# Kernel tuning notes

Hardware: AMD Instinct MI355X
Metric: run time of the kernel (lower is better)

Reference implementation:

```python
import jax, jax.numpy as jnp
import numpy as np

N_TOKENS, D_MODEL, D_HIDDEN, TOPK = 4096, 1024, 16384, 64


def setup_inputs() -> dict:
    key = jax.random.key(0)
    k0, k1, k2 = jax.random.split(key, 3)
    x = jax.random.normal(k0, (N_TOKENS, D_MODEL), dtype=jnp.float32)
    # kaiming_uniform_(a=sqrt(5)) -> bound = 1/sqrt(fan_in)
    lim_enc = 1.0 / np.sqrt(D_MODEL)
    W_enc = jax.random.uniform(k1, (D_MODEL, D_HIDDEN), jnp.float32, -lim_enc, lim_enc)
    b_enc = jnp.zeros((D_HIDDEN,), jnp.float32)
    lim_dec = 1.0 / np.sqrt(D_HIDDEN)
    W_dec = jax.random.uniform(k2, (D_HIDDEN, D_MODEL), jnp.float32, -lim_dec, lim_dec)
    # normalize_decoder=True: rows (one per feature) are unit-normalized in-place
    # under no_grad in torch, so we pre-normalize the parameter here.
    W_dec = W_dec / jnp.clip(jnp.linalg.norm(W_dec, axis=1, keepdims=True), 1e-8, None)
    b_dec = jnp.zeros((D_MODEL,), jnp.float32)
    return {"x": x, "W_enc": W_enc, "b_enc": b_enc, "W_dec": W_dec, "b_dec": b_dec, "k": TOPK}


def reference(x, W_enc, b_enc, W_dec, b_dec, k):
    # encode
    pre = x @ W_enc + b_enc                     # [N, d_hidden]
    # ReLU activation (config in ('relu','topk'))
    z = jax.nn.relu(pre)
    # TopK on |z| along feature dim, scatter original values back
    _, idx = jax.lax.top_k(jnp.abs(z), k)        # [N, k]
    rows = jnp.arange(z.shape[0])[:, None]       # [N, 1]
    z_sparse = jnp.zeros_like(z).at[rows, idx].set(jnp.take_along_axis(z, idx, axis=-1))
    # decode (W_dec rows are already unit-norm; torch re-normalizes under no_grad)
    y = z_sparse @ W_dec + b_dec                # [N, d_model]
    return y
```

## Files before the change

### kernel.cpp

```cpp
#include <hip/hip_runtime.h>

typedef unsigned short ushort_t;
typedef unsigned short ushort8 __attribute__((ext_vector_type(8)));
typedef __bf16 bf16x8 __attribute__((ext_vector_type(8)));
typedef float f32x4 __attribute__((ext_vector_type(4)));

#define N_TOKENS 4096
#define D_MODEL  1024
#define D_HIDDEN 16384
#define TOPK     64
#define DELTA    0.03f
#define RCAP     128

__device__ __forceinline__ float bf2f(ushort_t u) {
  union { unsigned u; float f; } c; c.u = ((unsigned)u) << 16; return c.f;
}
__device__ __forceinline__ ushort_t f2bf(float f) {
  union { float f; unsigned u; } c; c.f = f;
  unsigned x = c.u;
  unsigned r = (x + 0x7FFFu + ((x >> 16) & 1u)) >> 16;
  return (ushort_t)r;
}

typedef __attribute__((address_space(1))) void GV;
typedef __attribute__((address_space(3))) void LV;
__device__ __forceinline__ void llds16(const void* g, void* l) {
  __builtin_amdgcn_global_load_lds((GV*)g, (LV*)l, 16, 0, 0);
}

__global__ __launch_bounds__(256) void cast_x_kernel(
    const float* __restrict__ in, ushort_t* __restrict__ out) {
  const int i = (blockIdx.x * 256 + threadIdx.x) * 4;
  float4 v = *(const float4*)&in[i];
  ushort4 o;
  o.x = f2bf(v.x); o.y = f2bf(v.y); o.z = f2bf(v.z); o.w = f2bf(v.w);
  *(ushort4*)&out[i] = o;
}

__global__ __launch_bounds__(256) void cast_wdec_kernel(
    const float* __restrict__ in, ushort_t* __restrict__ out) {
  const int i = (blockIdx.x * 256 + threadIdx.x) * 8;
  float4 v0 = *(const float4*)&in[i];
  float4 v1 = *(const float4*)&in[i + 4];
  ushort8 o;
  o[0] = f2bf(v0.x); o[1] = f2bf(v0.y); o[2] = f2bf(v0.z); o[3] = f2bf(v0.w);
  o[4] = f2bf(v1.x); o[5] = f2bf(v1.y); o[6] = f2bf(v1.z); o[7] = f2bf(v1.w);
  *(ushort8*)&out[i] = o;
}

__global__ __launch_bounds__(256) void transpose_cast_kernel(
    const float* __restrict__ in, ushort_t* __restrict__ outb,
    float* __restrict__ out32) {
  __shared__ float tile[64][68];
  const int tid = threadIdx.x;
  const int n0 = blockIdx.x * 64;
  const int k0 = blockIdx.y * 64;
#pragma unroll
  for (int i = 0; i < 4; ++i) {
    int e = i * 256 + tid;
    int kk = e >> 4;
    int nn = (e & 15) * 4;
    float4 v = *(const float4*)&in[(size_t)(k0 + kk) * D_HIDDEN + n0 + nn];
    tile[kk][nn + 0] = v.x;
    tile[kk][nn + 1] = v.y;
    tile[kk][nn + 2] = v.z;
    tile[kk][nn + 3] = v.w;
  }
  __syncthreads();
#pragma unroll
  for (int i = 0; i < 4; ++i) {
    int e = i * 256 + tid;
    int nn = e >> 4;
    int kk = (e & 15) * 4;
    float4 f;
    f.x = tile[kk + 0][nn];
    f.y = tile[kk + 1][nn];
    f.z = tile[kk + 2][nn];
    f.w = tile[kk + 3][nn];
    *(float4*)&out32[(size_t)(n0 + nn) * D_MODEL + k0 + kk] = f;
    ushort4 b;
    b.x = f2bf(f.x); b.y = f2bf(f.y); b.z = f2bf(f.z); b.w = f2bf(f.w);
    *(ushort4*)&outb[(size_t)(n0 + nn) * D_MODEL + k0 + kk] = b;
  }
}

__global__ __launch_bounds__(256) void encode_gemm(
    const ushort_t* __restrict__ X, const ushort_t* __restrict__ WT,
    const float* __restrict__ benc, ushort_t* __restrict__ Z) {
  __shared__ ushort_t As[128 * 32];
  __shared__ ushort_t Bs[128 * 32];
  const int tid  = threadIdx.x;
  const int wave = tid >> 6, lane = tid & 63;
  const int m0 = blockIdx.y * 128;
  const int n0 = blockIdx.x * 128;
  const int wm = (wave >> 1) * 64;
  const int wn = (wave & 1) * 64;
  const int lr = lane >> 2;
  const int lk = (lane & 3) * 8;

  f32x4 acc[4][4];
#pragma unroll
  for (int i = 0; i < 4; ++i)
#pragma unroll
    for (int j = 0; j < 4; ++j) acc[i][j] = (f32x4){0.f, 0.f, 0.f, 0.f};

  for (int k0 = 0; k0 < D_MODEL; k0 += 32) {
    __syncthreads();
#pragma unroll
    for (int c = 0; c < 2; ++c) {
      const int chunk = c * 4 + wave;
      const int m = chunk * 16 + lr;
      llds16(&X [(size_t)(m0 + m) * D_MODEL + k0 + lk], &As[chunk * 512]);
      llds16(&WT[(size_t)(n0 + m) * D_MODEL + k0 + lk], &Bs[chunk * 512]);
    }
    __syncthreads();
    bf16x8 af[4], bfr[4];
#pragma unroll
    for (int t = 0; t < 4; ++t) {
      af[t]  = *(const bf16x8*)&As[(wm + t * 16 + (lane & 15)) * 32 + (lane >> 4) * 8];
      bfr[t] = *(const bf16x8*)&Bs[(wn + t * 16 + (lane & 15)) * 32 + (lane >> 4) * 8];
    }
#pragma unroll
    for (int mt = 0; mt < 4; ++mt)
#pragma unroll
      for (int nt = 0; nt < 4; ++nt)
        acc[mt][nt] = __builtin_amdgcn_mfma_f32_16x16x32_bf16(
            af[mt], bfr[nt], acc[mt][nt], 0, 0, 0);
  }

  const int col_base = n0 + wn + (lane & 15);
  const int row_base = m0 + wm + (lane >> 4) * 4;
#pragma unroll
  for (int nt = 0; nt < 4; ++nt) {
    const float bias = benc[col_base + nt * 16];
#pragma unroll
    for (int mt = 0; mt < 4; ++mt) {
#pragma unroll
      for (int r = 0; r < 4; ++r) {
        float v = fmaxf(acc[mt][nt][r] + bias, 0.0f);
        Z[(size_t)(row_base + mt * 16 + r) * D_HIDDEN + col_base + nt * 16] = f2bf(v);
      }
    }
  }
}

__global__ __launch_bounds__(256) void topk_refine_kernel(
    const ushort_t* __restrict__ Z, const float* __restrict__ x32,
    const float* __restrict__ WT32, const float* __restrict__ benc,
    float* __restrict__ vals, int* __restrict__ idxs) {
  __shared__ int    hist[2048];
  __shared__ float  cval[1024];
  __shared__ int    cidx[1024];
  __shared__ int    tsum[256], suff[256];
  __shared__ float  xrow[1024];
  __shared__ int    ridx[RCAP];
  __shared__ double rex[RCAP];
  __shared__ int    sTbin, sAbove, selCount, candCount, refCount;
  __shared__ float  sV64;
  const int tid  = threadIdx.x;
  const int wave = tid >> 6, lane = tid & 63;
  const int row  = blockIdx.x;
  const ushort_t* zr = Z + (size_t)row * D_HIDDEN;

  float v[64];
#pragma unroll
  for (int i = 0; i < 8; ++i) {
    ushort8 w = *(const ushort8*)&zr[i * 2048 + tid * 8];
#pragma unroll
    for (int u = 0; u < 8; ++u) v[i * 8 + u] = bf2f(w[u]);
  }
#define VIDX(i) (((i) >> 3) * 2048 + tid * 8 + ((i) & 7))

  *(float4*)&xrow[tid * 4] = *(const float4*)&x32[(size_t)row * D_MODEL + tid * 4];
#pragma unroll
  for (int i = 0; i < 8; ++i) hist[tid * 8 + i] = 0;
  if (tid == 0) { sTbin = -1; selCount = 0; candCount = 0; refCount = 0; }
  __syncthreads();
#pragma unroll
  for (int i = 0; i < 64; ++i)
    if (v[i] > 0.0f) atomicAdd(&hist[__float_as_uint(v[i]) >> 20], 1);
  __syncthreads();
  int s = 0;
#pragma unroll
  for (int i = 0; i < 8; ++i) s += hist[tid * 8 + i];
  tsum[tid] = s;
  __syncthreads();
  if (tid == 0) {
    int run = 0;
    for (int t = 255; t >= 0; --t) { suff[t] = run; run += tsum[t]; }
  }
  __syncthreads();
  {
    int cum = suff[tid];
    for (int key = tid * 8 + 7; key >= tid * 8; --key) {
      int h = hist[key];
      if (cum < TOPK && cum + h >= TOPK) { sTbin = key; sAbove = cum; }
      cum += h;
    }
  }
  __syncthreads();
  const int Tbin = sTbin, nAbove = sAbove;

  if (Tbin < 0) {
#pragma unroll
    for (int i = 0; i < 64; ++i) {
      if (v[i] > 0.0f) {
        int p = atomicAdd(&selCount, 1);
        if (p < TOPK) { vals[row * 64 + p] = v[i]; idxs[row * 64 + p] = VIDX(i); }
      }
    }
    __syncthreads();
    for (int p2 = min(selCount, TOPK) + tid; p2 < TOPK; p2 += 256) {
      vals[row * 64 + p2] = 0.0f; idxs[row * 64 + p2] = 0;
    }
    return;
  }

#pragma unroll
  for (int i = 0; i < 64; ++i) {
    if (v[i] > 0.0f && (int)(__float_as_uint(v[i]) >> 20) == Tbin) {
      int c = atomicAdd(&candCount, 1);
      if (c < 1024) { cval[c] = v[i]; cidx[c] = VIDX(i); }
    }
  }
  __syncthreads();
  {
    const int r  = TOPK - nAbove;
    const int nc = min(candCount, 1024);
    for (int j = tid; j < nc; j += 256) {
      float vj = cval[j]; int ij = cidx[j];
      int rank = 0;
      for (int j2 = 0; j2 < nc; ++j2) {
        float v2 = cval[j2];
        rank += (v2 > vj) || (v2 == vj && cidx[j2] < ij);
      }
      if (rank == r - 1) sV64 = vj;
    }
  }
  __syncthreads();
  const float v64 = sV64;

#pragma unroll
  for (int i = 0; i < 64; ++i) {
    if (v[i] > v64 + DELTA) {
      int p = atomicAdd(&selCount, 1);
      vals[row * 64 + p] = v[i];
      idxs[row * 64 + p] = VIDX(i);
    } else if (v[i] >= v64 - DELTA) {
      int c = atomicAdd(&refCount, 1);
      if (c < RCAP) ridx[c] = VIDX(i);
    }
  }
  __syncthreads();
  const int nS = selCount;
  const int nR = min(refCount, RCAP);
  const int rNeed = TOPK - nS;

  float xr[16];
#pragma unroll
  for (int q = 0; q < 16; ++q) xr[q] = xrow[lane * 16 + q];
  for (int c = wave; c < nR; c += 4) {
    const int j = ridx[c];
    const float* wr = &WT32[(size_t)j * D_MODEL];
    double p0 = 0.0, p1 = 0.0;
#pragma unroll
    for (int q = 0; q < 2; ++q) {
      const float4 wa = *(const float4*)&wr[lane * 16 + q * 8];
      const float4 wb = *(const float4*)&wr[lane * 16 + q * 8 + 4];
      p0 += (double)xr[q * 8 + 0] * wa.x + (double)xr[q * 8 + 1] * wa.y
          + (double)xr[q * 8 + 2] * wa.z + (double)xr[q * 8 + 3] * wa.w;
      p1 += (double)xr[q * 8 + 4] * wb.x + (double)xr[q * 8 + 5] * wb.y
          + (double)xr[q * 8 + 6] * wb.z + (double)xr[q * 8 + 7] * wb.w;
    }
    double part = p0 + p1;
#pragma unroll
    for (int off = 32; off > 0; off >>= 1) part += __shfl_down(part, off, 64);
    if (lane == 0) {
      double d = part + (double)benc[j];
      rex[c] = d > 0.0 ? d : 0.0;
    }
  }
  __syncthreads();

  for (int c = tid; c < nR; c += 256) {
    double vc = rex[c]; int ic = ridx[c];
    int rank = 0;
    for (int c2 = 0; c2 < nR; ++c2) {
      double v2 = rex[c2];
      rank += (v2 > vc) || (v2 == vc && ridx[c2] < ic);
    }
    if (rank < rNeed) {
      int p = atomicAdd(&selCount, 1);
      vals[row * 64 + p] = (float)vc;
      idxs[row * 64 + p] = ic;
    }
  }
}

__global__ __launch_bounds__(256) void decode_kernel(
    const float* __restrict__ vals, const int* __restrict__ idxs,
    const ushort_t* __restrict__ Wdec_bf, const float* __restrict__ bdec,
    float* __restrict__ Y) {
  __shared__ float sv[2][TOPK];
  __shared__ int   si[2][TOPK];
  const int tid = threadIdx.x;
  const int r0  = blockIdx.x * 2;
  if (tid < 128) {
    int rr = tid >> 6, jj = tid & 63;
    sv[rr][jj] = vals[(r0 + rr) * 64 + jj];
    si[rr][jj] = idxs[(r0 + rr) * 64 + jj];
  }
  __syncthreads();
  const int rr  = tid >> 7;
  const int c0  = (tid & 127) * 8;
  const int row = r0 + rr;
  float4 b0 = *(const float4*)&bdec[c0];
  float4 b1 = *(const float4*)&bdec[c0 + 4];
  float a[8] = {b0.x, b0.y, b0.z, b0.w, b1.x, b1.y, b1.z, b1.w};
#pragma unroll 8
  for (int j = 0; j < TOPK; ++j) {
    const float vj = sv[rr][j];
    ushort8 w = *(const ushort8*)&Wdec_bf[(size_t)si[rr][j] * D_MODEL + c0];
#pragma unroll
    for (int u = 0; u < 8; ++u) a[u] += vj * bf2f(w[u]);
  }
  *(float4*)&Y[(size_t)row * D_MODEL + c0]     = (float4){a[0], a[1], a[2], a[3]};
  *(float4*)&Y[(size_t)row * D_MODEL + c0 + 4] = (float4){a[4], a[5], a[6], a[7]};
}

extern "C" void kernel_launch(void* const* d_in, const int* in_sizes, int n_in,
                              void* d_out, int out_size, void* d_ws, size_t ws_size,
                              hipStream_t stream) {
  const float* x     = (const float*)d_in[0];
  const float* W_enc = (const float*)d_in[1];
  const float* b_enc = (const float*)d_in[2];
  const float* W_dec = (const float*)d_in[3];
  const float* b_dec = (const float*)d_in[4];

  const size_t WT_BYTES   = (size_t)D_HIDDEN * D_MODEL * sizeof(ushort_t);
  const size_t WT32_BYTES = (size_t)D_HIDDEN * D_MODEL * sizeof(float);
  const size_t XB_BYTES   = (size_t)N_TOKENS * D_MODEL * sizeof(ushort_t);
  const size_t V_BYTES    = (size_t)N_TOKENS * TOPK * sizeof(float);
  const size_t FIXED      = WT_BYTES + WT32_BYTES + XB_BYTES + 2 * V_BYTES;

  int chunk_rows = 4096;
  while (chunk_rows > 128 &&
         FIXED + (size_t)chunk_rows * D_HIDDEN * sizeof(ushort_t) > ws_size)
    chunk_rows >>= 1;

  char* ws = (char*)d_ws;
  ushort_t* WT   = (ushort_t*)ws;
  float*    WT32 = (float*)(ws + WT_BYTES);
  ushort_t* XB   = (ushort_t*)(ws + WT_BYTES + WT32_BYTES);
  float*    vals = (float*)(ws + WT_BYTES + WT32_BYTES + XB_BYTES);
  int*      idxs = (int*)(ws + WT_BYTES + WT32_BYTES + XB_BYTES + V_BYTES);
  ushort_t* Z    = (ushort_t*)(ws + FIXED);
  float*    Y    = (float*)d_out;

  cast_x_kernel<<<dim3(N_TOKENS * D_MODEL / 1024), 256, 0, stream>>>(x, XB);
  transpose_cast_kernel<<<dim3(D_HIDDEN / 64, D_MODEL / 64), 256, 0, stream>>>(
      W_enc, WT, WT32);

  for (int r0 = 0; r0 < N_TOKENS; r0 += chunk_rows) {
    encode_gemm<<<dim3(D_HIDDEN / 128, chunk_rows / 128), 256, 0, stream>>>(
        XB + (size_t)r0 * D_MODEL, WT, b_enc, Z);
    topk_refine_kernel<<<dim3(chunk_rows), 256, 0, stream>>>(
        Z, x + (size_t)r0 * D_MODEL, WT32, b_enc,
        vals + (size_t)r0 * TOPK, idxs + (size_t)r0 * TOPK);
  }

  cast_wdec_kernel<<<dim3(D_HIDDEN * D_MODEL / (256 * 8)), 256, 0, stream>>>(W_dec, WT);

  decode_kernel<<<dim3(N_TOKENS / 2), 256, 0, stream>>>(vals, idxs, WT, b_dec, Y);
}
```

Measured before the change: 554.7 us.

## Shrink top-k refine kernel LDS and registers with privatized 512-bin histogram

Keeps the Z row packed as bf16 in registers instead of expanding it to 64 floats. The histogram now keys on bf16 bits with 512 bins and 8 privatized copies, and the serial prefix scan is replaced by a wave shuffle scan. Candidate, refinement and histogram buffers are aliased into one LDS array, and the row of x is read straight from global memory. Together with launch_bounds(256,8) this aims to raise occupancy and cut atomic contention. The tradeoff is that candidates are capped at 512 and the bins are coarser, so more values may land in the threshold bin.

```diff
diff --git a/kernel.cpp b/kernel.cpp
--- a/kernel.cpp
+++ b/kernel.cpp
@@ -11,6 +11,7 @@
 #define TOPK     64
 #define DELTA    0.03f
 #define RCAP     128
+#define CANDCAP  512
 
 __device__ __forceinline__ float bf2f(ushort_t u) {
   union { unsigned u; float f; } c; c.u = ((unsigned)u) << 16; return c.f;
@@ -144,71 +145,81 @@
   }
 }
 
-__global__ __launch_bounds__(256) void topk_refine_kernel(
+__global__ __launch_bounds__(256, 8) void topk_refine_kernel(
     const ushort_t* __restrict__ Z, const float* __restrict__ x32,
     const float* __restrict__ WT32, const float* __restrict__ benc,
     float* __restrict__ vals, int* __restrict__ idxs) {
-  __shared__ int    hist[2048];
-  __shared__ float  cval[1024];
-  __shared__ int    cidx[1024];
-  __shared__ int    tsum[256], suff[256];
-  __shared__ float  xrow[1024];
-  __shared__ int    ridx[RCAP];
-  __shared__ double rex[RCAP];
-  __shared__ int    sTbin, sAbove, selCount, candCount, refCount;
-  __shared__ float  sV64;
+  __shared__ int hist[512 * 9 + 32];
+  float*  cval = (float*)hist;
+  int*    cidx = (int*)hist + 512;
+  int*    ridx = (int*)hist + 1024;
+  double* rex  = (double*)((int*)hist + 1156);
+  __shared__ int   wtot[4];
+  __shared__ int   sTbin, sAbove, selCount, candCount, refCount;
+  __shared__ float sV64;
+
   const int tid  = threadIdx.x;
   const int wave = tid >> 6, lane = tid & 63;
   const int row  = blockIdx.x;
   const ushort_t* zr = Z + (size_t)row * D_HIDDEN;
 
-  float v[64];
-#pragma unroll
-  for (int i = 0; i < 8; ++i) {
-    ushort8 w = *(const ushort8*)&zr[i * 2048 + tid * 8];
-#pragma unroll
-    for (int u = 0; u < 8; ++u) v[i * 8 + u] = bf2f(w[u]);
-  }
-#define VIDX(i) (((i) >> 3) * 2048 + tid * 8 + ((i) & 7))
-
-  *(float4*)&xrow[tid * 4] = *(const float4*)&x32[(size_t)row * D_MODEL + tid * 4];
-#pragma unroll
-  for (int i = 0; i < 8; ++i) hist[tid * 8 + i] = 0;
+  ushort8 u8v[8];
+#pragma unroll
+  for (int i = 0; i < 8; ++i) u8v[i] = *(const ushort8*)&zr[i * 2048 + tid * 8];
+#define ZIDX(i, j) ((i) * 2048 + tid * 8 + (j))
+
+  for (int k = tid; k < 512 * 9; k += 256) hist[k] = 0;
   if (tid == 0) { sTbin = -1; selCount = 0; candCount = 0; refCount = 0; }
   __syncthreads();
-#pragma unroll
-  for (int i = 0; i < 64; ++i)
-    if (v[i] > 0.0f) atomicAdd(&hist[__float_as_uint(v[i]) >> 20], 1);
-  __syncthreads();
-  int s = 0;
-#pragma unroll
-  for (int i = 0; i < 8; ++i) s += hist[tid * 8 + i];
-  tsum[tid] = s;
-  __syncthreads();
-  if (tid == 0) {
-    int run = 0;
-    for (int t = 255; t >= 0; --t) { suff[t] = run; run += tsum[t]; }
-  }
-  __syncthreads();
-  {
-    int cum = suff[tid];
-    for (int key = tid * 8 + 7; key >= tid * 8; --key) {
-      int h = hist[key];
-      if (cum < TOPK && cum + h >= TOPK) { sTbin = key; sAbove = cum; }
-      cum += h;
-    }
-  }
+
+  const int cpy = lane & 7;
+#pragma unroll
+  for (int i = 0; i < 8; ++i)
+#pragma unroll
+    for (int j = 0; j < 8; ++j) {
+      ushort_t w = u8v[i][j];
+      if (w) atomicAdd(&hist[((int)(w >> 6)) * 9 + cpy], 1);
+    }
+  __syncthreads();
+
+  int h0 = 0, h1 = 0;
+#pragma unroll
+  for (int c = 0; c < 8; ++c) {
+    int cc = (tid + c) & 7;
+    h0 += hist[(2 * tid) * 9 + cc];
+    h1 += hist[(2 * tid + 1) * 9 + cc];
+  }
+  const int s = h0 + h1;
+  int x = s;
+#pragma unroll
+  for (int off = 1; off < 64; off <<= 1) {
+    int y = __shfl_down(x, off, 64);
+    if (lane + off < 64) x += y;
+  }
+  if (lane == 0) wtot[wave] = x;
+  __syncthreads();
+  int cross = 0;
+  if (wave < 3) cross += wtot[3];
+  if (wave < 2) cross += wtot[2];
+  if (wave < 1) cross += wtot[1];
+  const int Sexc = cross + x - s;
+  if (Sexc < TOPK && Sexc + h1 >= TOPK) { sTbin = 2 * tid + 1; sAbove = Sexc; }
+  const int c0 = Sexc + h1;
+  if (c0 < TOPK && c0 + h0 >= TOPK) { sTbin = 2 * tid; sAbove = c0; }
   __syncthreads();
   const int Tbin = sTbin, nAbove = sAbove;
 
   if (Tbin < 0) {
 #pragma unroll
-    for (int i = 0; i < 64; ++i) {
-      if (v[i] > 0.0f) {
-        int p = atomicAdd(&selCount, 1);
-        if (p < TOPK) { vals[row * 64 + p] = v[i]; idxs[row * 64 + p] = VIDX(i); }
-      }
-    }
+    for (int i = 0; i < 8; ++i)
+#pragma unroll
+      for (int j = 0; j < 8; ++j) {
+        ushort_t w = u8v[i][j];
+        if (w) {
+          int p = atomicAdd(&selCount, 1);
+          if (p < TOPK) { vals[row * 64 + p] = bf2f(w); idxs[row * 64 + p] = ZIDX(i, j); }
+        }
+      }
     __syncthreads();
     for (int p2 = min(selCount, TOPK) + tid; p2 < TOPK; p2 += 256) {
       vals[row * 64 + p2] = 0.0f; idxs[row * 64 + p2] = 0;
@@ -217,16 +228,19 @@
   }
 
 #pragma unroll
-  for (int i = 0; i < 64; ++i) {
-    if (v[i] > 0.0f && (int)(__float_as_uint(v[i]) >> 20) == Tbin) {
-      int c = atomicAdd(&candCount, 1);
-      if (c < 1024) { cval[c] = v[i]; cidx[c] = VIDX(i); }
-    }
-  }
+  for (int i = 0; i < 8; ++i)
+#pragma unroll
+    for (int j = 0; j < 8; ++j) {
+      ushort_t w = u8v[i][j];
+      if (w && (int)(w >> 6) == Tbin) {
+        int c = atomicAdd(&candCount, 1);
+        if (c < CANDCAP) { cval[c] = bf2f(w); cidx[c] = ZIDX(i, j); }
+      }
+    }
   __syncthreads();
   {
     const int r  = TOPK - nAbove;
-    const int nc = min(candCount, 1024);
+    const int nc = min(candCount, CANDCAP);
     for (int j = tid; j < nc; j += 256) {
       float vj = cval[j]; int ij = cidx[j];
       int rank = 0;
@@ -241,24 +255,33 @@
   const float v64 = sV64;
 
 #pragma unroll
-  for (int i = 0; i < 64; ++i) {
-    if (v[i] > v64 + DELTA) {
-      int p = atomicAdd(&selCount, 1);
-      vals[row * 64 + p] = v[i];
-      idxs[row * 64 + p] = VIDX(i);
-    } else if (v[i] >= v64 - DELTA) {
-      int c = atomicAdd(&refCount, 1);
-      if (c < RCAP) ridx[c] = VIDX(i);
-    }
-  }
+  for (int i = 0; i < 8; ++i)
+#pragma unroll
+    for (int j = 0; j < 8; ++j) {
+      ushort_t w = u8v[i][j];
+      if (!w) continue;
+      float v = bf2f(w);
+      if (v > v64 + DELTA) {
+        int p = atomicAdd(&selCount, 1);
+        vals[row * 64 + p] = v;
+        idxs[row * 64 + p] = ZIDX(i, j);
+      } else if (v >= v64 - DELTA) {
+        int c = atomicAdd(&refCount, 1);
+        if (c < RCAP) ridx[c] = ZIDX(i, j);
+      }
+    }
   __syncthreads();
   const int nS = selCount;
   const int nR = min(refCount, RCAP);
   const int rNeed = TOPK - nS;
 
   float xr[16];
-#pragma unroll
-  for (int q = 0; q < 16; ++q) xr[q] = xrow[lane * 16 + q];
+  {
+    const float* xrb = &x32[(size_t)row * D_MODEL + lane * 16];
+#pragma unroll
+    for (int q = 0; q < 4; ++q)
+      *(float4*)&xr[q * 4] = *(const float4*)&xrb[q * 4];
+  }
   for (int c = wave; c < nR; c += 4) {
     const int j = ridx[c];
     const float* wr = &WT32[(size_t)j * D_MODEL];
```

After: 876.9 us. 58.1% more time.
